# Kernel tuning notes

Measured on AMD Instinct MI355X. Metric: run time of the kernel, lower is better.

## Reference

```python
import jax, jax.numpy as jnp
import numpy as np

D_MODEL = 1024
N_HEADS = 16
D_K = D_MODEL // N_HEADS
B, S = 4, 2048
NEG = -1e9


def setup_inputs() -> dict:
    key = jax.random.key(0)
    ks = jax.random.split(key, 9)
    scale = 1.0 / np.sqrt(D_MODEL)
    x = jax.random.normal(ks[0], (B, S, D_MODEL), dtype=jnp.float32)
    mask = jnp.tril(jnp.ones((S, S), dtype=jnp.int32))  # causal lower-triangular
    Wq = jax.random.normal(ks[1], (D_MODEL, D_MODEL), dtype=jnp.float32) * scale
    Wk = jax.random.normal(ks[2], (D_MODEL, D_MODEL), dtype=jnp.float32) * scale
    Wv = jax.random.normal(ks[3], (D_MODEL, D_MODEL), dtype=jnp.float32) * scale
    Wo = jax.random.normal(ks[4], (D_MODEL, D_MODEL), dtype=jnp.float32) * scale
    bq = jnp.zeros((D_MODEL,), dtype=jnp.float32)
    bk = jnp.zeros((D_MODEL,), dtype=jnp.float32)
    bv = jnp.zeros((D_MODEL,), dtype=jnp.float32)
    bo = jnp.zeros((D_MODEL,), dtype=jnp.float32)
    return {"x": x, "mask": mask, "Wq": Wq, "bq": bq, "Wk": Wk, "bk": bk,
            "Wv": Wv, "bv": bv, "Wo": Wo, "bo": bo}


def reference(x, mask, Wq, bq, Wk, bk, Wv, bv, Wo, bo):
    b, s, _ = x.shape
    # nn.Linear: y = x @ W.T + b
    Q = x @ Wq.T + bq
    K = x @ Wk.T + bk
    V = x @ Wv.T + bv
    # [b, h, s, d_k]
    Q = Q.reshape(b, s, N_HEADS, D_K).transpose(0, 2, 1, 3)
    K = K.reshape(b, s, N_HEADS, D_K).transpose(0, 2, 1, 3)
    V = V.reshape(b, s, N_HEADS, D_K).transpose(0, 2, 1, 3)
    score = jnp.einsum('bhqd,bhkd->bhqk', Q, K) / jnp.sqrt(jnp.float32(D_K))
    score = jnp.where(mask == 0, jnp.float32(NEG), score)
    attn = jax.nn.softmax(score, axis=-1)
    out = jnp.einsum('bhqk,bhkd->bhqd', attn, V)
    out = out.transpose(0, 2, 1, 3).reshape(b, s, D_MODEL)
    return out @ Wo.T + bo
```

## Files before the change

### kernel.cpp

```cpp
#include <hip/hip_runtime.h>
#include <hip/hip_bf16.h>
#include <stdint.h>

typedef __bf16 bf16x8 __attribute__((ext_vector_type(8)));
typedef float  f32x4  __attribute__((ext_vector_type(4)));

#define B_   4
#define S_   2048
#define DM   1024
#define H_   16
#define DK   64
#define M_TOT 8192

__device__ __forceinline__ void gld16(const __bf16* g, char* l) {
    __builtin_amdgcn_global_load_lds(
        (const __attribute__((address_space(1))) void*)g,
        (__attribute__((address_space(3))) void*)l,
        16, 0, 0);
}

__global__ __launch_bounds__(256)
void cvt_f32_bf16(const float* __restrict__ in, __bf16* __restrict__ out, int n) {
    int i = (blockIdx.x * 256 + threadIdx.x) * 8;
    if (i >= n) return;
    float4 a = *(const float4*)(in + i);
    float4 c = *(const float4*)(in + i + 4);
    bf16x8 o;
    o[0] = (__bf16)a.x; o[1] = (__bf16)a.y; o[2] = (__bf16)a.z; o[3] = (__bf16)a.w;
    o[4] = (__bf16)c.x; o[5] = (__bf16)c.y; o[6] = (__bf16)c.z; o[7] = (__bf16)c.w;
    *(bf16x8*)(out + i) = o;
}

__global__ __launch_bounds__(256)
void cvt4_w(const float* __restrict__ w0, const float* __restrict__ w1,
            const float* __restrict__ w2, const float* __restrict__ w3,
            __bf16* __restrict__ out) {
    const int z = blockIdx.z;
    const float* in = (z == 0) ? w0 : (z == 1) ? w1 : (z == 2) ? w2 : w3;
    int i = (blockIdx.x * 256 + threadIdx.x) * 8;
    float4 a = *(const float4*)(in + i);
    float4 c = *(const float4*)(in + i + 4);
    bf16x8 o;
    o[0] = (__bf16)a.x; o[1] = (__bf16)a.y; o[2] = (__bf16)a.z; o[3] = (__bf16)a.w;
    o[4] = (__bf16)c.x; o[5] = (__bf16)c.y; o[6] = (__bf16)c.z; o[7] = (__bf16)c.w;
    *(bf16x8*)(out + (size_t)z * (DM * DM) + i) = o;
}

__device__ __forceinline__ void gemm_core(const __bf16* __restrict__ A,
                                          const __bf16* __restrict__ W,
                                          int m0, int n0,
                                          f32x4 (&acc)[4][4]) {
    __shared__ __bf16 As[128 * 64];
    __shared__ __bf16 Bs[128 * 64];
    const int tid  = threadIdx.x;
    const int wid  = tid >> 6;
    const int lane = tid & 63;
    const int ln15 = lane & 15, lg = lane >> 4;
    const int wr = (wid >> 1) * 64;
    const int wc = (wid & 1) * 64;

    const int r0 = tid >> 3;
    const int sc = ((tid & 7) ^ (r0 & 7)) * 8;
    char* la = (char*)As + wid * 1024;
    char* lb = (char*)Bs + wid * 1024;
    const int rsw = ln15 & 7;

    for (int k0 = 0; k0 < DM; k0 += 64) {
#pragma unroll
        for (int i = 0; i < 4; ++i) {
            gld16(A + (size_t)(m0 + r0 + i * 32) * DM + k0 + sc, la + i * 4096);
            gld16(W + (size_t)(n0 + r0 + i * 32) * DM + k0 + sc, lb + i * 4096);
        }
        __syncthreads();
#pragma unroll
        for (int kk = 0; kk < 2; ++kk) {
            bf16x8 af[4], bfr[4];
#pragma unroll
            for (int m = 0; m < 4; ++m)
                af[m] = *(const bf16x8*)&As[(wr + m * 16 + ln15) * 64 + (((kk * 4 + lg) ^ rsw) * 8)];
#pragma unroll
            for (int n = 0; n < 4; ++n)
                bfr[n] = *(const bf16x8*)&Bs[(wc + n * 16 + ln15) * 64 + (((kk * 4 + lg) ^ rsw) * 8)];
#pragma unroll
            for (int m = 0; m < 4; ++m)
#pragma unroll
                for (int n = 0; n < 4; ++n)
                    acc[m][n] = __builtin_amdgcn_mfma_f32_16x16x32_bf16(af[m], bfr[n], acc[m][n], 0, 0, 0);
        }
        __syncthreads();
    }
}

__global__ __launch_bounds__(256)
void gemm_qkv_kernel(const __bf16* __restrict__ Xb,
                     const __bf16* __restrict__ Wq, const __bf16* __restrict__ Wk,
                     const __bf16* __restrict__ Wv,
                     const float* __restrict__ bq, const float* __restrict__ bk,
                     const float* __restrict__ bv,
                     __bf16* __restrict__ Qb, __bf16* __restrict__ Kb,
                     __bf16* __restrict__ Vt) {
    const int z = blockIdx.z;
    const __bf16* W   = (z == 0) ? Wq : (z == 1) ? Wk : Wv;
    const float* bias = (z == 0) ? bq : (z == 1) ? bk : bv;
    const int m0 = blockIdx.x * 128, n0 = blockIdx.y * 128;

    f32x4 acc[4][4] = {};
    gemm_core(Xb, W, m0, n0, acc);

    const int tid = threadIdx.x, wid = tid >> 6, lane = tid & 63;
    const int ln15 = lane & 15, lg = lane >> 4;
    const int wr = (wid >> 1) * 64, wc = (wid & 1) * 64;
    const float oscl = (z == 0) ? 0.18033688f : 1.0f;

    if (z < 2) {
        __bf16* out = (z == 0) ? Qb : Kb;
#pragma unroll
        for (int ni = 0; ni < 4; ++ni) {
            int col = n0 + wc + ni * 16 + ln15;
            int h = col >> 6, d = col & 63;
            float bval = bias[col];
#pragma unroll
            for (int mi = 0; mi < 4; ++mi)
#pragma unroll
                for (int r = 0; r < 4; ++r) {
                    int row = m0 + wr + mi * 16 + lg * 4 + r;
                    int b = row >> 11, s = row & 2047;
                    out[(((size_t)(b * H_ + h)) * S_ + s) * DK + d] =
                        (__bf16)((acc[mi][ni][r] + bval) * oscl);
                }
        }
    } else {
#pragma unroll
        for (int ni = 0; ni < 4; ++ni) {
            int col = n0 + wc + ni * 16 + ln15;
            int h = col >> 6, d = col & 63;
            float bval = bias[col];
#pragma unroll
            for (int mi = 0; mi < 4; ++mi)
#pragma unroll
                for (int r = 0; r < 4; ++r) {
                    int row = m0 + wr + mi * 16 + lg * 4 + r;
                    int b = row >> 11, s = row & 2047;
                    Vt[(((size_t)(b * H_ + h)) * DK + d) * S_ + s] =
                        (__bf16)(acc[mi][ni][r] + bval);
                }
        }
    }
}

__global__ __launch_bounds__(256)
void gemm_out_kernel(const __bf16* __restrict__ Ab, const __bf16* __restrict__ Wo,
                     const float* __restrict__ bo, float* __restrict__ out) {
    const int m0 = blockIdx.x * 128, n0 = blockIdx.y * 128;
    f32x4 acc[4][4] = {};
    gemm_core(Ab, Wo, m0, n0, acc);

    const int tid = threadIdx.x, wid = tid >> 6, lane = tid & 63;
    const int ln15 = lane & 15, lg = lane >> 4;
    const int wr = (wid >> 1) * 64, wc = (wid & 1) * 64;
#pragma unroll
    for (int ni = 0; ni < 4; ++ni) {
        int col = n0 + wc + ni * 16 + ln15;
        float bval = bo[col];
#pragma unroll
        for (int mi = 0; mi < 4; ++mi)
#pragma unroll
            for (int r = 0; r < 4; ++r) {
                int row = m0 + wr + mi * 16 + lg * 4 + r;
                out[(size_t)row * DM + col] = acc[mi][ni][r] + bval;
            }
    }
}

__global__ __launch_bounds__(512)
void attn_kernel(const __bf16* __restrict__ Qb, const __bf16* __restrict__ Kb,
                 const __bf16* __restrict__ Vt, __bf16* __restrict__ AO) {
    __shared__ __bf16 Ks[2][128 * 64];
    __shared__ __bf16 Vs[2][64 * 128];

    const int tid = threadIdx.x, wid = tid >> 6, lane = tid & 63;
    const int ln15 = lane & 15, lg = lane >> 4;
    const int bh = blockIdx.x;
    const int p  = blockIdx.y;
    const size_t base = (size_t)bh * (S_ * DK);
    const int b = bh >> 4, h = bh & 15;

    const int krow = wid * 8 + (lane >> 3);
    const int kswz = ((lane & 7) ^ (krow & 7)) * 8;
    const int vrow = wid * 4 + (lane >> 4);
    const int vswz = ((lane & 15) ^ (vrow & 15)) * 8;
    const int swz  = (ln15 & 7) << 3;

    const __bf16* kgb = Kb + base;
    const __bf16* vgb = Vt + base;

    auto stage = [&](int buf, int kt) {
        char* dk = (char*)Ks + buf * 16384 + wid * 1024;
        char* dv = (char*)Vs + buf * 16384 + wid * 1024;
        gld16(kgb + (size_t)(kt * 128 + krow) * DK + kswz, dk);
        gld16(kgb + (size_t)(kt * 128 + krow + 64) * DK + kswz, dk + 8192);
        gld16(vgb + (size_t)vrow * S_ + kt * 128 + vswz, dv);
        gld16(vgb + (size_t)(vrow + 32) * S_ + kt * 128 + vswz, dv + 8192);
    };

    bf16x8 ones;
#pragma unroll
    for (int j = 0; j < 8; ++j) ones[j] = (__bf16)1.0f;

#pragma unroll
    for (int ph = 0; ph < 2; ++ph) {
        const int qb   = ph ? p : 15 - p;
        const int last = qb;
        const int qr0  = qb * 128 + wid * 16 + ln15;

        bf16x8 qf[2];
        {
            int q0 = qr0;
            qf[0] = *(const bf16x8*)&Qb[base + (size_t)q0 * DK + lg * 8];
            qf[1] = *(const bf16x8*)&Qb[base + (size_t)q0 * DK + 32 + lg * 8];
        }

        f32x4 acc[4] = {};
        f32x4 lacc = {};

        __builtin_amdgcn_s_barrier();
        stage(0, 0);
        asm volatile("s_waitcnt vmcnt(0)" ::: "memory");
        __builtin_amdgcn_s_barrier();
        __builtin_amdgcn_sched_barrier(0);

        for (int kt = 0; kt <= last; ++kt) {
            const int cur = kt & 1;
            if (kt < last) stage(cur ^ 1, kt + 1);

            const __bf16* ksb = &Ks[cur][0];
            const __bf16* vsb = &Vs[cur][0];

            f32x4 z[8] = {};
            __builtin_amdgcn_s_setprio(1);
#pragma unroll
            for (int cb = 0; cb < 8; ++cb)
#pragma unroll
                for (int kk = 0; kk < 2; ++kk) {
                    bf16x8 kf = *(const bf16x8*)&ksb[(cb * 16 + ln15) * 64 + ((kk * 32 + lg * 8) ^ swz)];
                    z[cb] = __builtin_amdgcn_mfma_f32_16x16x32_bf16(kf, qf[kk], z[cb], 0, 0, 0);
                }
            __builtin_amdgcn_s_setprio(0);

            if (kt == last) {
                const int kcb = kt * 128 + lg * 4;
#pragma unroll
                for (int cb = 0; cb < 8; ++cb)
#pragma unroll
                    for (int r = 0; r < 4; ++r)
                        if (kcb + cb * 16 + r > qr0) z[cb][r] = -3e8f;
            }

            uint32_t a0[8], b0[8];
#pragma unroll
            for (int cb = 0; cb < 8; ++cb) {
                float e0 = exp2f(z[cb][0]), e1 = exp2f(z[cb][1]);
                float e2 = exp2f(z[cb][2]), e3 = exp2f(z[cb][3]);
                asm("v_cvt_pk_bf16_f32 %0, %1, %2" : "=v"(a0[cb]) : "v"(e0), "v"(e1));
                asm("v_cvt_pk_bf16_f32 %0, %1, %2" : "=v"(b0[cb]) : "v"(e2), "v"(e3));
            }

            union U8 { uint32_t u[4]; bf16x8 v; };
            bf16x8 pa[4];
#pragma unroll
            for (int ks = 0; ks < 4; ++ks) {
                uint32_t x = a0[2 * ks], y = a0[2 * ks + 1];
                asm("v_permlane32_swap_b32 %0, %1" : "+v"(x), "+v"(y));
                asm("v_permlane16_swap_b32 %0, %1" : "+v"(x), "+v"(y));
                uint32_t p2 = b0[2 * ks], q2 = b0[2 * ks + 1];
                asm("v_permlane32_swap_b32 %0, %1" : "+v"(p2), "+v"(q2));
                asm("v_permlane16_swap_b32 %0, %1" : "+v"(p2), "+v"(q2));
                U8 f; f.u[0] = x; f.u[1] = p2; f.u[2] = y; f.u[3] = q2;
                pa[ks] = f.v;
            }

            __builtin_amdgcn_s_setprio(1);
#pragma unroll
            for (int ks = 0; ks < 4; ++ks) {
                lacc = __builtin_amdgcn_mfma_f32_16x16x32_bf16(pa[ks], ones, lacc, 0, 0, 0);
#pragma unroll
                for (int db = 0; db < 4; ++db) {
                    bf16x8 vf = *(const bf16x8*)&vsb[(db * 16 + ln15) * 128 + (((ks * 4 + lg) ^ ln15) * 8)];
                    acc[db] = __builtin_amdgcn_mfma_f32_16x16x32_bf16(pa[ks], vf, acc[db], 0, 0, 0);
                }
            }
            __builtin_amdgcn_s_setprio(0);

            if (kt < last) {
                asm volatile("s_waitcnt vmcnt(0)" ::: "memory");
                __builtin_amdgcn_s_barrier();
                __builtin_amdgcn_sched_barrier(0);
            }
        }

#pragma unroll
        for (int r = 0; r < 4; ++r) {
            float i0 = 1.f / lacc[r];
            int s0r = qb * 128 + wid * 16 + lg * 4 + r;
#pragma unroll
            for (int db = 0; db < 4; ++db)
                AO[((size_t)(b * S_ + s0r)) * DM + h * DK + db * 16 + ln15] = (__bf16)(acc[db][r] * i0);
        }
    }
}

extern "C" void kernel_launch(void* const* d_in, const int* in_sizes, int n_in,
                              void* d_out, int out_size, void* d_ws, size_t ws_size,
                              hipStream_t stream) {
    const float* x  = (const float*)d_in[0];
    const float* Wq = (const float*)d_in[2];
    const float* bq = (const float*)d_in[3];
    const float* Wk = (const float*)d_in[4];
    const float* bk = (const float*)d_in[5];
    const float* Wv = (const float*)d_in[6];
    const float* bv = (const float*)d_in[7];
    const float* Wo = (const float*)d_in[8];
    const float* bo = (const float*)d_in[9];
    float* out = (float*)d_out;

    char* ws = (char*)d_ws;
    __bf16* xb  = (__bf16*)ws;
    __bf16* wqb = (__bf16*)(ws + 16777216);
    __bf16* wkb = wqb + 1048576;
    __bf16* wvb = wkb + 1048576;
    __bf16* wob = wvb + 1048576;
    __bf16* Qb  = (__bf16*)(ws + 25165824);
    __bf16* Kb  = Qb + 8388608;
    __bf16* Vt  = Kb + 8388608;
    __bf16* AO  = xb;

    cvt_f32_bf16<<<4096, 256, 0, stream>>>(x, xb, M_TOT * DM);
    cvt4_w<<<dim3(512, 1, 4), 256, 0, stream>>>(Wq, Wk, Wv, Wo, wqb);

    gemm_qkv_kernel<<<dim3(64, 8, 3), 256, 0, stream>>>(xb, wqb, wkb, wvb,
                                                        bq, bk, bv, Qb, Kb, Vt);
    attn_kernel<<<dim3(64, 8), 512, 0, stream>>>(Qb, Kb, Vt, AO);
    gemm_out_kernel<<<dim3(64, 8), 256, 0, stream>>>(AO, wob, bo, out);
}
```

Measured before the change: 170.8 us.

## Widen QKV GEMM tile to 128x256 and merge fp32-to-bf16 conversion launches

The QKV projection GEMM now uses 512-thread blocks, each computing a 128x256 output tile with eight waves of 64x64. This halves the number of times each A (activation) tile is reloaded across the N dimension and raises the work per block. The two conversion kernels for x and the four weights are merged into one launch that picks its source by flat index, removing one kernel launch. The wider tile uses more LDS (48KB) and fewer blocks (768), which may lower occupancy and latency hiding.

```diff
diff --git a/kernel.cpp b/kernel.cpp
--- a/kernel.cpp
+++ b/kernel.cpp
@@ -20,30 +20,27 @@
 }
 
 __global__ __launch_bounds__(256)
-void cvt_f32_bf16(const float* __restrict__ in, __bf16* __restrict__ out, int n) {
+void cvt_all(const float* __restrict__ x,
+             const float* __restrict__ w0, const float* __restrict__ w1,
+             const float* __restrict__ w2, const float* __restrict__ w3,
+             __bf16* __restrict__ xb, __bf16* __restrict__ wb) {
     int i = (blockIdx.x * 256 + threadIdx.x) * 8;
-    if (i >= n) return;
-    float4 a = *(const float4*)(in + i);
-    float4 c = *(const float4*)(in + i + 4);
+    const float* in;
+    __bf16* out;
+    if (i < M_TOT * DM) {
+        in = x + i; out = xb + i;
+    } else {
+        int j = i - M_TOT * DM;
+        int w = j >> 20;
+        const float* ws4[4] = {w0, w1, w2, w3};
+        in = ws4[w] + (j & 1048575); out = wb + j;
+    }
+    float4 a = *(const float4*)in;
+    float4 c = *(const float4*)(in + 4);
     bf16x8 o;
     o[0] = (__bf16)a.x; o[1] = (__bf16)a.y; o[2] = (__bf16)a.z; o[3] = (__bf16)a.w;
     o[4] = (__bf16)c.x; o[5] = (__bf16)c.y; o[6] = (__bf16)c.z; o[7] = (__bf16)c.w;
-    *(bf16x8*)(out + i) = o;
-}
-
-__global__ __launch_bounds__(256)
-void cvt4_w(const float* __restrict__ w0, const float* __restrict__ w1,
-            const float* __restrict__ w2, const float* __restrict__ w3,
-            __bf16* __restrict__ out) {
-    const int z = blockIdx.z;
-    const float* in = (z == 0) ? w0 : (z == 1) ? w1 : (z == 2) ? w2 : w3;
-    int i = (blockIdx.x * 256 + threadIdx.x) * 8;
-    float4 a = *(const float4*)(in + i);
-    float4 c = *(const float4*)(in + i + 4);
-    bf16x8 o;
-    o[0] = (__bf16)a.x; o[1] = (__bf16)a.y; o[2] = (__bf16)a.z; o[3] = (__bf16)a.w;
-    o[4] = (__bf16)c.x; o[5] = (__bf16)c.y; o[6] = (__bf16)c.z; o[7] = (__bf16)c.w;
-    *(bf16x8*)(out + (size_t)z * (DM * DM) + i) = o;
+    *(bf16x8*)out = o;
 }
 
 __device__ __forceinline__ void gemm_core(const __bf16* __restrict__ A,
@@ -91,7 +88,53 @@
     }
 }
 
-__global__ __launch_bounds__(256)
+__device__ __forceinline__ void gemm_core_wide(const __bf16* __restrict__ A,
+                                               const __bf16* __restrict__ W,
+                                               int m0, int n0,
+                                               f32x4 (&acc)[4][4]) {
+    __shared__ __bf16 As[128 * 64];
+    __shared__ __bf16 Bs[256 * 64];
+    const int tid  = threadIdx.x;
+    const int wid  = tid >> 6;
+    const int lane = tid & 63;
+    const int ln15 = lane & 15, lg = lane >> 4;
+    const int wr = (wid >> 2) * 64;
+    const int wc = (wid & 3) * 64;
+
+    const int r0 = tid >> 3;
+    const int sc = ((tid & 7) ^ (r0 & 7)) * 8;
+    char* la = (char*)As + wid * 1024;
+    char* lb = (char*)Bs + wid * 1024;
+    const int rsw = ln15 & 7;
+
+    for (int k0 = 0; k0 < DM; k0 += 64) {
+#pragma unroll
+        for (int i = 0; i < 2; ++i)
+            gld16(A + (size_t)(m0 + r0 + i * 64) * DM + k0 + sc, la + i * 8192);
+#pragma unroll
+        for (int i = 0; i < 4; ++i)
+            gld16(W + (size_t)(n0 + r0 + i * 64) * DM + k0 + sc, lb + i * 8192);
+        __syncthreads();
+#pragma unroll
+        for (int kk = 0; kk < 2; ++kk) {
+            bf16x8 af[4], bfr[4];
+#pragma unroll
+            for (int m = 0; m < 4; ++m)
+                af[m] = *(const bf16x8*)&As[(wr + m * 16 + ln15) * 64 + (((kk * 4 + lg) ^ rsw) * 8)];
+#pragma unroll
+            for (int n = 0; n < 4; ++n)
+                bfr[n] = *(const bf16x8*)&Bs[(wc + n * 16 + ln15) * 64 + (((kk * 4 + lg) ^ rsw) * 8)];
+#pragma unroll
+            for (int m = 0; m < 4; ++m)
+#pragma unroll
+                for (int n = 0; n < 4; ++n)
+                    acc[m][n] = __builtin_amdgcn_mfma_f32_16x16x32_bf16(af[m], bfr[n], acc[m][n], 0, 0, 0);
+        }
+        __syncthreads();
+    }
+}
+
+__global__ __launch_bounds__(512)
 void gemm_qkv_kernel(const __bf16* __restrict__ Xb,
                      const __bf16* __restrict__ Wq, const __bf16* __restrict__ Wk,
                      const __bf16* __restrict__ Wv,
@@ -102,14 +145,14 @@
     const int z = blockIdx.z;
     const __bf16* W   = (z == 0) ? Wq : (z == 1) ? Wk : Wv;
     const float* bias = (z == 0) ? bq : (z == 1) ? bk : bv;
-    const int m0 = blockIdx.x * 128, n0 = blockIdx.y * 128;
+    const int m0 = blockIdx.x * 128, n0 = blockIdx.y * 256;
 
     f32x4 acc[4][4] = {};
-    gemm_core(Xb, W, m0, n0, acc);
+    gemm_core_wide(Xb, W, m0, n0, acc);
 
     const int tid = threadIdx.x, wid = tid >> 6, lane = tid & 63;
     const int ln15 = lane & 15, lg = lane >> 4;
-    const int wr = (wid >> 1) * 64, wc = (wid & 1) * 64;
+    const int wr = (wid >> 2) * 64, wc = (wid & 3) * 64;
     const float oscl = (z == 0) ? 0.18033688f : 1.0f;
 
     if (z < 2) {
@@ -334,10 +377,9 @@
     __bf16* Vt  = Kb + 8388608;
     __bf16* AO  = xb;
 
-    cvt_f32_bf16<<<4096, 256, 0, stream>>>(x, xb, M_TOT * DM);
-    cvt4_w<<<dim3(512, 1, 4), 256, 0, stream>>>(Wq, Wk, Wv, Wo, wqb);
-
-    gemm_qkv_kernel<<<dim3(64, 8, 3), 256, 0, stream>>>(xb, wqb, wkb, wvb,
+    cvt_all<<<6144, 256, 0, stream>>>(x, Wq, Wk, Wv, Wo, xb, wqb);
+
+    gemm_qkv_kernel<<<dim3(64, 4, 3), 512, 0, stream>>>(xb, wqb, wkb, wvb,
                                                         bq, bk, bv, Qb, Kb, Vt);
     attn_kernel<<<dim3(64, 8), 512, 0, stream>>>(Qb, Kb, Vt, AO);
     gemm_out_kernel<<<dim3(64, 8), 256, 0, stream>>>(AO, wob, bo, out);
```

Result: no change. 174.1 us (+2.0%).
